# Kernel tuning notes

Hardware: AMD Instinct MI355X
Metric: run time of the kernel (lower is better)

The kernel has to match this reference:

```python
import jax, jax.numpy as jnp
import numpy as np

DIM, HEADS, HD = 256, 8, 32
WS, GT, SR = 8, 1, 2
B_, H0, W0 = 4, 128, 128
SCALE = HD ** -0.5


def _bilinear_up_align(x, s):
    # x: (B, C, h, w) -> (B, C, h*s, w*s), bilinear, align_corners=True (matches torch)
    B, C, h, w = x.shape
    oh, ow = h * s, w * s
    def coords(n, o):
        pos = jnp.arange(o, dtype=jnp.float32) * ((n - 1) / (o - 1))
        i0 = jnp.clip(jnp.floor(pos).astype(jnp.int32), 0, n - 2)
        t = pos - i0.astype(jnp.float32)
        return i0, t
    y0, ty = coords(h, oh)
    x0, tx = coords(w, ow)
    top = x[:, :, y0, :] * (1 - ty)[:, None] + x[:, :, y0 + 1, :] * ty[:, None]
    return top[:, :, :, x0] * (1 - tx) + top[:, :, :, x0 + 1] * tx


def _layernorm(x, w, b, eps=1e-5):
    mu = x.mean(-1, keepdims=True)
    var = x.var(-1, keepdims=True)
    return (x - mu) * jax.lax.rsqrt(var + eps) * w + b


def setup_inputs() -> dict:
    key = jax.random.key(0)
    ks = jax.random.split(key, 8)
    w = lambda k, shape: jax.random.normal(k, shape, jnp.float32) * 0.02
    return {
        "x": jax.random.normal(ks[0], (B_, H0 * W0, DIM), jnp.float32),
        "gt": jax.random.normal(ks[1], (B_, H0 // WS, W0 // WS, GT, DIM), jnp.float32),
        "q_w": w(ks[2], (DIM, DIM)), "q_b": jnp.zeros((DIM,), jnp.float32),
        "kv_w": w(ks[3], (2 * DIM, DIM)), "kv_b": jnp.zeros((2 * DIM,), jnp.float32),
        "sr_w": w(ks[4], (DIM, DIM, SR, SR)), "sr_b": jnp.zeros((DIM,), jnp.float32),
        "norm_w": jnp.ones((DIM,), jnp.float32), "norm_b": jnp.zeros((DIM,), jnp.float32),
        "proj_w": w(ks[5], (DIM, DIM)), "proj_b": jnp.zeros((DIM,), jnp.float32),
        "H": H0, "W": W0,
    }


def reference(x, gt, q_w, q_b, kv_w, kv_b, sr_w, sr_b, norm_w, norm_b, proj_w, proj_b, H, W):
    Bb, Np, C = x.shape
    nH, nW = H // WS, W // WS  # H, W multiples of WS -> no padding branch
    xm = x.reshape(Bb, H, W, C)
    # window partition -> (B, WS*WS, C), B = Bb*nH*nW
    xw = xm.reshape(Bb, nH, WS, nW, WS, C).transpose(0, 1, 3, 2, 4, 5).reshape(-1, WS * WS, C)
    g = gt.reshape(-1, GT, C)  # gt grid already matches (nH, nW)
    skip = g
    xc = jnp.concatenate([g, xw], axis=1)  # (B, N, C), N = GT + WS*WS
    B, N, _ = xc.shape
    q = (xc @ q_w.T + q_b).reshape(B, N, HEADS, HD).transpose(0, 2, 1, 3)  # (B,h,N,d)
    # spatial-reduction KV branch (sr_ratio > 1, gt_num != 0)
    x_ = xw.transpose(0, 2, 1).reshape(B, C, WS, WS)
    x_ = _bilinear_up_align(x_, SR)  # (B, C, WS*SR, WS*SR)
    x_ = jax.lax.conv_general_dilated(
        x_, sr_w, (SR, SR), "VALID",
        dimension_numbers=("NCHW", "OIHW", "NCHW")) + sr_b[None, :, None, None]  # (B,C,WS,WS)
    x_ = _layernorm(x_.reshape(B, C, -1).transpose(0, 2, 1), norm_w, norm_b)
    x_ = jnp.concatenate([g, x_], axis=1)  # (B, N, C)
    kv = (x_ @ kv_w.T + kv_b).reshape(B, -1, 2, HEADS, HD).transpose(2, 0, 3, 1, 4)
    k, v = kv[0], kv[1]  # (B,h,N,d)
    attn = jax.nn.softmax(jnp.einsum("bhnd,bhmd->bhnm", q, k) * SCALE, axis=-1)
    out = jnp.einsum("bhnm,bhmd->bhnd", attn, v).transpose(0, 2, 1, 3).reshape(B, N, C)
    out = out @ proj_w.T + proj_b
    gt_out = out[:, :GT, :]
    xo = out[:, GT:, :].reshape(Bb, nH, nW, WS, WS, C)
    xo = xo.transpose(0, 1, 3, 2, 4, 5).reshape(Bb, H, W, C)  # window reverse
    return xo.reshape(Bb, H * W, C), gt_out, skip
```

## Files before the change

kernel.cpp:

```cpp
#include <hip/hip_runtime.h>

typedef __attribute__((ext_vector_type(4))) float f32x4;
typedef __attribute__((ext_vector_type(8))) float f32x8;
typedef __attribute__((ext_vector_type(8))) short bf16x8;
typedef __attribute__((ext_vector_type(2))) uint u32x2;

#define SCALE_ 0.17677669529663687f

__device__ __forceinline__ float bf2f(ushort u){
  union { unsigned i; float f; } v; v.i = ((unsigned)u) << 16; return v.f;
}
__device__ __forceinline__ ushort f2bf(float f){
  union { float f; unsigned i; } v; v.f = f;
  unsigned r = v.i + 0x7fffu + ((v.i >> 16) & 1u);
  return (ushort)(r >> 16);
}
__device__ __forceinline__ void gl16(const void* g, const ushort* l) {
  __builtin_amdgcn_global_load_lds((const __attribute__((address_space(1))) uint*)g,
                                   (__attribute__((address_space(3))) uint*)l, 16, 0, 0);
}

__global__ __launch_bounds__(256) void k_prep(const float* __restrict__ x,
    const float* __restrict__ gt, const float* __restrict__ qw,
    const float* __restrict__ kvw, const float* __restrict__ pw,
    const float* __restrict__ srw, ushort* __restrict__ xc,
    ushort* __restrict__ xkv, float* __restrict__ out2,
    ushort* __restrict__ wq, ushort* __restrict__ wkv,
    ushort* __restrict__ wpr, ushort* __restrict__ wcv)
{
  int blk = blockIdx.x;
  int tid = threadIdx.x;
  if (blk >= 16640) {
    int i = (blk - 16640) * 256 + tid;
    if (i < 65536)            wq[i] = f2bf(qw[i]);
    else if (i < 196608)      wkv[i - 65536] = f2bf(kvw[i - 65536]);
    else if (i < 262144)      wpr[i - 196608] = f2bf(pw[i - 196608]);
    else {
      int j = i - 262144;
      int o = j >> 10, t = (j >> 8) & 3, cc = j & 255;
      wcv[j] = f2bf(srw[o * 1024 + cc * 4 + t]);
    }
    return;
  }
  int row = blk * 4 + (tid >> 6);
  int c4 = (tid & 63) * 4;
  int wi = row / 65, n = row - wi * 65;
  if (n == 0) {
    float4 g4 = *(const float4*)(gt + (size_t)wi * 256 + c4);
    uint lo = (uint)f2bf(g4.x) | ((uint)f2bf(g4.y) << 16);
    uint hi = (uint)f2bf(g4.z) | ((uint)f2bf(g4.w) << 16);
    u32x2 pk = {lo, hi};
    *(u32x2*)(xc  + (size_t)row * 256 + c4) = pk;
    *(u32x2*)(xkv + (size_t)row * 256 + c4) = pk;
    *(float4*)(out2 + (size_t)wi * 256 + c4) = g4;
  } else {
    int s = n - 1, r = s >> 3, cc = s & 7;
    int b = wi >> 8, wh = (wi >> 4) & 15, ww = wi & 15;
    int hw = (wh * 8 + r) * 128 + ww * 8 + cc;
    float4 v4 = *(const float4*)(x + ((size_t)b * 16384 + hw) * 256 + c4);
    uint lo = (uint)f2bf(v4.x) | ((uint)f2bf(v4.y) << 16);
    uint hi = (uint)f2bf(v4.z) | ((uint)f2bf(v4.w) << 16);
    u32x2 pk = {lo, hi};
    *(u32x2*)(xc + (size_t)row * 256 + c4) = pk;
  }
}

template<int N>
__global__ __launch_bounds__(256) void k_gemm2(const ushort* __restrict__ A,
    const ushort* __restrict__ W, const float* __restrict__ bias,
    ushort* __restrict__ C)
{
  constexpr int K = 256;
  __shared__ __align__(16) ushort As[2][128 * 64];
  __shared__ __align__(16) ushort Bs[2][128 * 64];
  int lin = blockIdx.y * gridDim.x + blockIdx.x;
  int qq = (gridDim.x * gridDim.y) >> 3;
  int sw2 = (lin & 7) * qq + (lin >> 3);
  int m0 = (sw2 / gridDim.x) * 128, n0 = (sw2 % gridDim.x) * 128;
  int tid = threadIdx.x, lane = tid & 63;
  int wave = tid >> 6;
  int lm = lane & 15, kg = lane >> 4;
  int wr = wave >> 1, wc = wave & 1;

  const char* Ab = (const char*)A + (size_t)m0 * (K * 2);
  const char* Bb = (const char*)W + (size_t)n0 * (K * 2);

  auto stage = [&](int buf, int kt) {
#pragma unroll
    for (int j = 0; j < 4; ++j) {
      int c = j * 256 + tid;
      int row = c >> 3, slot = c & 7;
      int srcoff = row * (K * 2) + kt * 128 + ((slot * 16) ^ ((row & 7) << 4));
      gl16(Ab + srcoff, (const ushort*)((const char*)As[buf] + c * 16));
      gl16(Bb + srcoff, (const ushort*)((const char*)Bs[buf] + c * 16));
    }
  };

  f32x4 acc[4][4];
  f32x4 zero = {0.f, 0.f, 0.f, 0.f};
#pragma unroll
  for (int a = 0; a < 4; ++a)
#pragma unroll
    for (int b = 0; b < 4; ++b) acc[a][b] = zero;

  stage(0, 0);
  __syncthreads();
#pragma unroll
  for (int t = 0; t < 4; ++t) {
    int cur = t & 1;
    if (t < 3) stage(cur ^ 1, t + 1);
#pragma unroll
    for (int s = 0; s < 2; ++s) {
      int sw = (lm & 7) << 4;
      bf16x8 af[4], bw[4];
#pragma unroll
      for (int mi = 0; mi < 4; ++mi) {
        int row = wr * 64 + mi * 16 + lm;
        af[mi] = *(const bf16x8*)((const char*)As[cur] + row * 128 + ((s * 64 + kg * 16) ^ sw));
      }
#pragma unroll
      for (int ni = 0; ni < 4; ++ni) {
        int row = wc * 64 + ni * 16 + lm;
        bw[ni] = *(const bf16x8*)((const char*)Bs[cur] + row * 128 + ((s * 64 + kg * 16) ^ sw));
      }
#pragma unroll
      for (int mi = 0; mi < 4; ++mi)
#pragma unroll
        for (int ni = 0; ni < 4; ++ni)
          acc[mi][ni] = __builtin_amdgcn_mfma_f32_16x16x32_bf16(af[mi], bw[ni], acc[mi][ni], 0, 0, 0);
    }
    __syncthreads();
  }

  int rbase = m0 + wr * 64 + kg * 4;
#pragma unroll
  for (int ni = 0; ni < 4; ++ni) {
    int col = n0 + wc * 64 + ni * 16 + lm;
    float bv = bias[col];
#pragma unroll
    for (int mi = 0; mi < 4; ++mi) {
#pragma unroll
      for (int r = 0; r < 4; ++r)
        C[(size_t)(rbase + mi * 16 + r) * N + col] = f2bf(acc[mi][ni][r] + bv);
    }
  }
}

__global__ __launch_bounds__(256) void k_gemm_out(const ushort* __restrict__ A,
    const ushort* __restrict__ W, const float* __restrict__ bias,
    float* __restrict__ out)
{
  constexpr int K = 256;
  __shared__ __align__(16) ushort As[2][128 * 64];
  __shared__ __align__(16) ushort Bs[2][128 * 64];
  int lin = blockIdx.y * gridDim.x + blockIdx.x;
  int qq = (gridDim.x * gridDim.y) >> 3;
  int sw2 = (lin & 7) * qq + (lin >> 3);
  int m0 = (sw2 / gridDim.x) * 128, n0 = (sw2 % gridDim.x) * 128;
  int tid = threadIdx.x, lane = tid & 63;
  int wave = tid >> 6;
  int lm = lane & 15, kg = lane >> 4;
  int wr = wave >> 1, wc = wave & 1;

  const char* Ab = (const char*)A + (size_t)m0 * (K * 2);
  const char* Bb = (const char*)W + (size_t)n0 * (K * 2);

  auto stage = [&](int buf, int kt) {
#pragma unroll
    for (int j = 0; j < 4; ++j) {
      int c = j * 256 + tid;
      int row = c >> 3, slot = c & 7;
      int srcoff = row * (K * 2) + kt * 128 + ((slot * 16) ^ ((row & 7) << 4));
      gl16(Ab + srcoff, (const ushort*)((const char*)As[buf] + c * 16));
      gl16(Bb + srcoff, (const ushort*)((const char*)Bs[buf] + c * 16));
    }
  };

  f32x4 acc[4][4];
  f32x4 zero = {0.f, 0.f, 0.f, 0.f};
#pragma unroll
  for (int a = 0; a < 4; ++a)
#pragma unroll
    for (int b = 0; b < 4; ++b) acc[a][b] = zero;

  stage(0, 0);
  __syncthreads();
#pragma unroll
  for (int t = 0; t < 4; ++t) {
    int cur = t & 1;
    if (t < 3) stage(cur ^ 1, t + 1);
#pragma unroll
    for (int s = 0; s < 2; ++s) {
      int sw = (lm & 7) << 4;
      bf16x8 af[4], bw[4];
#pragma unroll
      for (int mi = 0; mi < 4; ++mi) {
        int row = wr * 64 + mi * 16 + lm;
        af[mi] = *(const bf16x8*)((const char*)As[cur] + row * 128 + ((s * 64 + kg * 16) ^ sw));
      }
#pragma unroll
      for (int ni = 0; ni < 4; ++ni) {
        int row = wc * 64 + ni * 16 + lm;
        bw[ni] = *(const bf16x8*)((const char*)Bs[cur] + row * 128 + ((s * 64 + kg * 16) ^ sw));
      }
#pragma unroll
      for (int mi = 0; mi < 4; ++mi)
#pragma unroll
        for (int ni = 0; ni < 4; ++ni)
          acc[mi][ni] = __builtin_amdgcn_mfma_f32_16x16x32_bf16(af[mi], bw[ni], acc[mi][ni], 0, 0, 0);
    }
    __syncthreads();
  }

  int rbase = m0 + wr * 64 + kg * 4;
#pragma unroll
  for (int mi = 0; mi < 4; ++mi) {
#pragma unroll
    for (int r = 0; r < 4; ++r) {
      int g = rbase + mi * 16 + r;
      int wi2 = g / 65;
      int n = g - wi2 * 65;
      size_t dstrow;
      if (n == 0) {
        dstrow = (size_t)(16777216 >> 8) + wi2;
      } else {
        int s = n - 1;
        int b = wi2 >> 8, wh = (wi2 >> 4) & 15, ww = wi2 & 15;
        int r2 = s >> 3, cc = s & 7;
        dstrow = (size_t)(b << 14) + (wh * 8 + r2) * 128 + ww * 8 + cc;
      }
      float* dst = out + dstrow * 256;
#pragma unroll
      for (int ni = 0; ni < 4; ++ni) {
        int col = n0 + wc * 64 + ni * 16 + lm;
        dst[col] = acc[mi][ni][r] + bias[col];
      }
    }
  }
}

__global__ __launch_bounds__(512) void k_conv(const ushort* __restrict__ xc,
    const ushort* __restrict__ wconv, ushort* __restrict__ cconv)
{
  __shared__ ushort U[2][64 * 256];
  int wi = blockIdx.x;
  int tid = threadIdx.x, wave = tid >> 6, lane = tid & 63;
  int lm = lane & 15, kg = lane >> 4;
  const ushort* src = xc + (size_t)(wi * 65 + 1) * 256;
  f32x4 acc[4][2];
  f32x4 zero = {0.f, 0.f, 0.f, 0.f};
#pragma unroll
  for (int a = 0; a < 4; a++)
#pragma unroll
    for (int b = 0; b < 2; b++) acc[a][b] = zero;

  int cb = (tid & 31) * 8;
  int sg = tid >> 5;

  auto build = [&](int t, ushort* Ub) {
    int dy = t >> 1, dx = t & 1;
    for (int s = sg; s < 64; s += 16) {
      int i = s >> 3, j = s & 7;
      int yy = 2 * i + dy, xx = 2 * j + dx;
      float py = yy * (7.0f / 15.0f); int iy = (int)py; if (iy > 6) iy = 6; float ty = py - iy;
      float px = xx * (7.0f / 15.0f); int ix = (int)px; if (ix > 6) ix = 6; float tx = px - ix;
      float w00 = (1.f - ty) * (1.f - tx), w01 = (1.f - ty) * tx;
      float w10 = ty * (1.f - tx), w11 = ty * tx;
      const ushort* p = src + (size_t)(iy * 8 + ix) * 256 + cb;
      bf16x8 p00 = *(const bf16x8*)(p);
      bf16x8 p01 = *(const bf16x8*)(p + 256);
      bf16x8 p10 = *(const bf16x8*)(p + 2048);
      bf16x8 p11 = *(const bf16x8*)(p + 2304);
      bf16x8 o8;
#pragma unroll
      for (int jj = 0; jj < 8; jj++) {
        float v = w00 * bf2f((ushort)p00[jj]) + w01 * bf2f((ushort)p01[jj])
                + w10 * bf2f((ushort)p10[jj]) + w11 * bf2f((ushort)p11[jj]);
        o8[jj] = (short)f2bf(v);
      }
      int byteoff = s * 512 + ((2 * cb) ^ ((s & 7) << 4));
      *(bf16x8*)((char*)Ub + byteoff) = o8;
    }
  };

  build(0, U[0]);
  __syncthreads();
  for (int t = 0; t < 4; t++) {
    const ushort* Ub = U[t & 1];
    const ushort* wc = wconv + t * 256;
    for (int kk = 0; kk < 256; kk += 32) {
      int kb = kk + kg * 8;
      bf16x8 afr[4];
#pragma unroll
      for (int mi = 0; mi < 4; mi++) {
        int srow = mi * 16 + lm;
        int off = (srow * 512 + 2 * kb) ^ ((srow & 7) << 4);
        afr[mi] = *(const bf16x8*)((const char*)Ub + off);
      }
#pragma unroll
      for (int ni = 0; ni < 2; ni++) {
        bf16x8 b = *(const bf16x8*)(wc + (size_t)(wave * 32 + ni * 16 + lm) * 1024 + kb);
#pragma unroll
        for (int mi = 0; mi < 4; mi++)
          acc[mi][ni] = __builtin_amdgcn_mfma_f32_16x16x32_bf16(afr[mi], b, acc[mi][ni], 0, 0, 0);
      }
    }
    if (t < 3) build(t + 1, U[(t + 1) & 1]);
    __syncthreads();
  }

#pragma unroll
  for (int mi = 0; mi < 4; mi++) {
    int row = wi * 64 + mi * 16 + kg * 4;
#pragma unroll
    for (int ni = 0; ni < 2; ni++) {
      int col = wave * 32 + ni * 16 + lm;
#pragma unroll
      for (int r = 0; r < 4; r++)
        cconv[(size_t)(row + r) * 256 + col] = f2bf(acc[mi][ni][r]);
    }
  }
}

__global__ __launch_bounds__(256) void k_ln(const ushort* __restrict__ cconv,
    const float* __restrict__ srb, const float* __restrict__ nw,
    const float* __restrict__ nb, ushort* __restrict__ xkv)
{
  int row = blockIdx.x * 4 + (threadIdx.x >> 6);
  int lane = threadIdx.x & 63;
  int c0 = lane * 4;
  u32x2 pk = *(const u32x2*)(cconv + (size_t)row * 256 + c0);
  float4 sb4 = *(const float4*)(srb + c0);
  float v0 = bf2f((ushort)(pk.x & 0xffffu)) + sb4.x;
  float v1 = bf2f((ushort)(pk.x >> 16))     + sb4.y;
  float v2 = bf2f((ushort)(pk.y & 0xffffu)) + sb4.z;
  float v3 = bf2f((ushort)(pk.y >> 16))     + sb4.w;
  float sum = v0 + v1 + v2 + v3;
  float sq  = v0 * v0 + v1 * v1 + v2 * v2 + v3 * v3;
#pragma unroll
  for (int off = 1; off < 64; off <<= 1) {
    sum += __shfl_xor(sum, off, 64);
    sq  += __shfl_xor(sq,  off, 64);
  }
  float mean = sum * (1.f / 256.f);
  float var = sq * (1.f / 256.f) - mean * mean;
  float rs = rsqrtf(var + 1e-5f);
  float4 nw4 = *(const float4*)(nw + c0);
  float4 nb4 = *(const float4*)(nb + c0);
  int wi = row >> 6, s = row & 63;
  ushort* o = xkv + (size_t)(wi * 65 + 1 + s) * 256 + c0;
  uint lo = (uint)f2bf((v0 - mean) * rs * nw4.x + nb4.x)
          | ((uint)f2bf((v1 - mean) * rs * nw4.y + nb4.y) << 16);
  uint hi = (uint)f2bf((v2 - mean) * rs * nw4.z + nb4.z)
          | ((uint)f2bf((v3 - mean) * rs * nw4.w + nb4.w) << 16);
  u32x2 opk = {lo, hi};
  *(u32x2*)o = opk;
}

__global__ __launch_bounds__(256) void k_attn(const ushort* __restrict__ q,
    const ushort* __restrict__ kv, ushort* __restrict__ att)
{
  __shared__ ushort smem[4][8064];
  int wi = blockIdx.x >> 1;
  int tid = threadIdx.x, wave = tid >> 6, lane = tid & 63;
  int h = (blockIdx.x & 1) * 4 + wave;
  int lm = lane & 15, kg = lane >> 4;
  ushort* plds = smem[wave];
  ushort* vt   = smem[wave] + 5760;

  size_t qbase  = (size_t)wi * 65 * 256 + (size_t)h * 32;
  size_t kvbase = (size_t)wi * 65 * 512 + (size_t)h * 32;

  for (int e = lane; e < 2080; e += 64) {
    int m = e >> 5, d = e & 31;
    vt[d * 72 + m] = kv[kvbase + (size_t)m * 512 + 256 + d];
  }

  bf16x8 akf[5], bqf[5];
#pragma unroll
  for (int i = 0; i < 5; i++) {
    akf[i] = *(const bf16x8*)(kv + kvbase + (size_t)(16 * i + lm) * 512 + kg * 8);
    bqf[i] = *(const bf16x8*)(q  + qbase  + (size_t)(16 * i + lm) * 256 + kg * 8);
  }

  f32x4 sc[5][5];
  f32x4 zero = {0.f, 0.f, 0.f, 0.f};
#pragma unroll
  for (int mi = 0; mi < 5; mi++)
#pragma unroll
    for (int nj = 0; nj < 5; nj++) sc[mi][nj] = zero;
#pragma unroll
  for (int mi = 0; mi < 5; mi++)
#pragma unroll
    for (int nj = 0; nj < 5; nj++)
      sc[mi][nj] = __builtin_amdgcn_mfma_f32_16x16x32_bf16(akf[mi], bqf[nj], sc[mi][nj], 0, 0, 0);

  const float C = SCALE_ * 1.4426950408889634f;
  float inv[5], p64b[5];
#pragma unroll
  for (int nj = 0; nj < 5; nj++) {
    float s4 = sc[4][nj][0];
    float mx = (kg == 0) ? s4 : -1e30f;
#pragma unroll
    for (int mi = 0; mi < 4; mi++)
#pragma unroll
      for (int r = 0; r < 4; r++) mx = fmaxf(mx, sc[mi][nj][r]);
    mx = fmaxf(mx, __shfl_xor(mx, 16, 64));
    mx = fmaxf(mx, __shfl_xor(mx, 32, 64));
    float sum = 0.f;
#pragma unroll
    for (int mi = 0; mi < 4; mi++)
#pragma unroll
      for (int r = 0; r < 4; r++) {
        float e = exp2f((sc[mi][nj][r] - mx) * C);
        sc[mi][nj][r] = e; sum += e;
      }
    float e4 = exp2f((s4 - mx) * C);
    sum += (kg == 0) ? e4 : 0.f;
    sum += __shfl_xor(sum, 16, 64);
    sum += __shfl_xor(sum, 32, 64);
    inv[nj] = 1.0f / sum;
    p64b[nj] = __shfl(e4, lm, 64);
  }

#pragma unroll
  for (int nj = 0; nj < 5; nj++) {
    int n = 16 * nj + lm;
#pragma unroll
    for (int mi = 0; mi < 4; mi++) {
      uint lo = (uint)f2bf(sc[mi][nj][0]) | ((uint)f2bf(sc[mi][nj][1]) << 16);
      uint hi = (uint)f2bf(sc[mi][nj][2]) | ((uint)f2bf(sc[mi][nj][3]) << 16);
      u32x2 pk = {lo, hi};
      *(u32x2*)(plds + n * 72 + 16 * mi + 4 * kg) = pk;
    }
  }

  f32x4 od[2][5];
#pragma unroll
  for (int dt = 0; dt < 2; dt++)
#pragma unroll
    for (int nj = 0; nj < 5; nj++) od[dt][nj] = zero;
#pragma unroll
  for (int c = 0; c < 2; c++) {
    bf16x8 av[2], bp[5];
#pragma unroll
    for (int dt = 0; dt < 2; dt++)
      av[dt] = *(const bf16x8*)(vt + (16 * dt + lm) * 72 + c * 32 + kg * 8);
#pragma unroll
    for (int nj = 0; nj < 5; nj++)
      bp[nj] = *(const bf16x8*)(plds + (16 * nj + lm) * 72 + c * 32 + kg * 8);
#pragma unroll
    for (int dt = 0; dt < 2; dt++)
#pragma unroll
      for (int nj = 0; nj < 5; nj++)
        od[dt][nj] = __builtin_amdgcn_mfma_f32_16x16x32_bf16(av[dt], bp[nj], od[dt][nj], 0, 0, 0);
  }
  float v64[8];
#pragma unroll
  for (int dt = 0; dt < 2; dt++)
#pragma unroll
    for (int r = 0; r < 4; r++)
      v64[dt * 4 + r] = bf2f(vt[(16 * dt + 4 * kg + r) * 72 + 64]);
#pragma unroll
  for (int dt = 0; dt < 2; dt++)
#pragma unroll
    for (int nj = 0; nj < 5; nj++)
#pragma unroll
      for (int r = 0; r < 4; r++)
        od[dt][nj][r] += v64[dt * 4 + r] * p64b[nj];

#pragma unroll
  for (int nj = 0; nj < 5; nj++) {
    int n = 16 * nj + lm;
    float scl = inv[nj];
#pragma unroll
    for (int dt = 0; dt < 2; dt++) {
      uint lo = (uint)f2bf(od[dt][nj][0] * scl) | ((uint)f2bf(od[dt][nj][1] * scl) << 16);
      uint hi = (uint)f2bf(od[dt][nj][2] * scl) | ((uint)f2bf(od[dt][nj][3] * scl) << 16);
      u32x2 pk = {lo, hi};
      *(u32x2*)(plds + n * 40 + 16 * dt + 4 * kg) = pk;
    }
  }
  size_t abase = (size_t)wi * 65 * 256 + (size_t)h * 32;
  for (int e = lane; e < 1040; e += 64) {
    int n = e >> 4, d2 = e & 15;
    *(uint*)(att + abase + (size_t)n * 256 + 2 * d2) = *(const uint*)(plds + n * 40 + 2 * d2);
  }
}

extern "C" void kernel_launch(void* const* d_in, const int* in_sizes, int n_in,
                              void* d_out, int out_size, void* d_ws, size_t ws_size,
                              hipStream_t stream)
{
  const float* x    = (const float*)d_in[0];
  const float* gt   = (const float*)d_in[1];
  const float* q_w  = (const float*)d_in[2];
  const float* q_b  = (const float*)d_in[3];
  const float* kv_w = (const float*)d_in[4];
  const float* kv_b = (const float*)d_in[5];
  const float* sr_w = (const float*)d_in[6];
  const float* sr_b = (const float*)d_in[7];
  const float* nw   = (const float*)d_in[8];
  const float* nb   = (const float*)d_in[9];
  const float* p_w  = (const float*)d_in[10];
  const float* p_b  = (const float*)d_in[11];
  (void)in_sizes; (void)n_in; (void)out_size;

  if (ws_size < 204996608u) return;
  char* ws = (char*)d_ws;
  ushort* xc  = (ushort*)(ws);
  ushort* qb  = (ushort*)(ws + 34078720);
  ushort* xkv = (ushort*)(ws + 68157440);
  ushort* kv  = (ushort*)(ws + 102236160);
  ushort* ccv = (ushort*)(ws + 170393600);
  ushort* wq  = (ushort*)(ws + 203948032);
  ushort* wkv = (ushort*)(ws + 204079104);
  ushort* wpr = (ushort*)(ws + 204341248);
  ushort* wcv = (ushort*)(ws + 204472320);

  float* out = (float*)d_out;
  float* out2 = out + 16777216 + 262144;

  k_prep<<<18688, 256, 0, stream>>>(x, gt, q_w, kv_w, p_w, sr_w,
                                    xc, xkv, out2, wq, wkv, wpr, wcv);
  k_gemm2<256><<<dim3(2, 520), 256, 0, stream>>>(xc, wq, q_b, qb);
  k_conv<<<1024, 512, 0, stream>>>(xc, wcv, ccv);
  k_ln<<<16384, 256, 0, stream>>>(ccv, sr_b, nw, nb, xkv);
  k_gemm2<512><<<dim3(4, 520), 256, 0, stream>>>(xkv, wkv, kv_b, kv);
  k_attn<<<2048, 256, 0, stream>>>(qb, kv, xc);
  k_gemm_out<<<dim3(2, 520), 256, 0, stream>>>(xc, wpr, p_b, out);
}
```

Baseline: 240.1 us.

## Restructure conv kernel to 256 threads with half-K stages and smaller LDS

The spatial-reduction conv kernel now runs with 4 waves instead of 8, each wave covering 64 output columns. The K loop is split into 8 half-width stages of 128 channels, so the double-buffered LDS tile shrinks from 64 KB to 32 KB, which should allow more blocks resident per CU. The bilinear build gives each thread one fixed spatial position and 32 contiguous channels, hoisting the coordinate math out of the loop. In exchange there are more syncthreads, more accumulator registers per thread, and a changed LDS swizzle.

```diff
diff --git a/kernel.cpp b/kernel.cpp
--- a/kernel.cpp
+++ b/kernel.cpp
@@ -1,7 +1,6 @@
 #include <hip/hip_runtime.h>
 
 typedef __attribute__((ext_vector_type(4))) float f32x4;
-typedef __attribute__((ext_vector_type(8))) float f32x8;
 typedef __attribute__((ext_vector_type(8))) short bf16x8;
 typedef __attribute__((ext_vector_type(2))) uint u32x2;
 
@@ -239,73 +238,84 @@
   }
 }
 
-__global__ __launch_bounds__(512) void k_conv(const ushort* __restrict__ xc,
+__global__ __launch_bounds__(256) void k_conv(const ushort* __restrict__ xc,
     const ushort* __restrict__ wconv, ushort* __restrict__ cconv)
 {
-  __shared__ ushort U[2][64 * 256];
+  __shared__ __align__(16) ushort U2[2][64 * 128];
   int wi = blockIdx.x;
   int tid = threadIdx.x, wave = tid >> 6, lane = tid & 63;
   int lm = lane & 15, kg = lane >> 4;
   const ushort* src = xc + (size_t)(wi * 65 + 1) * 256;
-  f32x4 acc[4][2];
+
+  f32x4 acc[4][4];
   f32x4 zero = {0.f, 0.f, 0.f, 0.f};
 #pragma unroll
   for (int a = 0; a < 4; a++)
 #pragma unroll
-    for (int b = 0; b < 2; b++) acc[a][b] = zero;
-
-  int cb = (tid & 31) * 8;
-  int sg = tid >> 5;
-
-  auto build = [&](int t, ushort* Ub) {
+    for (int b = 0; b < 4; b++) acc[a][b] = zero;
+
+  int bs = tid >> 2, cq = tid & 3;
+  int bi = bs >> 3, bj = bs & 7;
+  float py = (2 * bi) * (7.0f / 15.0f);
+  float px = (2 * bj) * (7.0f / 15.0f);
+
+  auto build = [&](int st, ushort* Ub) {
+    int t = st >> 1, h = st & 1;
     int dy = t >> 1, dx = t & 1;
-    for (int s = sg; s < 64; s += 16) {
-      int i = s >> 3, j = s & 7;
-      int yy = 2 * i + dy, xx = 2 * j + dx;
-      float py = yy * (7.0f / 15.0f); int iy = (int)py; if (iy > 6) iy = 6; float ty = py - iy;
-      float px = xx * (7.0f / 15.0f); int ix = (int)px; if (ix > 6) ix = 6; float tx = px - ix;
-      float w00 = (1.f - ty) * (1.f - tx), w01 = (1.f - ty) * tx;
-      float w10 = ty * (1.f - tx), w11 = ty * tx;
-      const ushort* p = src + (size_t)(iy * 8 + ix) * 256 + cb;
-      bf16x8 p00 = *(const bf16x8*)(p);
-      bf16x8 p01 = *(const bf16x8*)(p + 256);
-      bf16x8 p10 = *(const bf16x8*)(p + 2048);
-      bf16x8 p11 = *(const bf16x8*)(p + 2304);
+    float pyt = py + dy * (7.0f / 15.0f);
+    float pxt = px + dx * (7.0f / 15.0f);
+    int iy = (int)pyt; if (iy > 6) iy = 6; float ty = pyt - iy;
+    int ix = (int)pxt; if (ix > 6) ix = 6; float tx = pxt - ix;
+    float w00 = (1.f - ty) * (1.f - tx), w01 = (1.f - ty) * tx;
+    float w10 = ty * (1.f - tx), w11 = ty * tx;
+    const ushort* p = src + (size_t)(iy * 8 + ix) * 256 + h * 128 + cq * 32;
+#pragma unroll
+    for (int j = 0; j < 4; ++j) {
+      bf16x8 p00 = *(const bf16x8*)(p + j * 8);
+      bf16x8 p01 = *(const bf16x8*)(p + j * 8 + 256);
+      bf16x8 p10 = *(const bf16x8*)(p + j * 8 + 2048);
+      bf16x8 p11 = *(const bf16x8*)(p + j * 8 + 2304);
       bf16x8 o8;
 #pragma unroll
-      for (int jj = 0; jj < 8; jj++) {
-        float v = w00 * bf2f((ushort)p00[jj]) + w01 * bf2f((ushort)p01[jj])
-                + w10 * bf2f((ushort)p10[jj]) + w11 * bf2f((ushort)p11[jj]);
-        o8[jj] = (short)f2bf(v);
-      }
-      int byteoff = s * 512 + ((2 * cb) ^ ((s & 7) << 4));
-      *(bf16x8*)((char*)Ub + byteoff) = o8;
+      for (int e = 0; e < 8; ++e) {
+        float v = w00 * bf2f((ushort)p00[e]) + w01 * bf2f((ushort)p01[e])
+                + w10 * bf2f((ushort)p10[e]) + w11 * bf2f((ushort)p11[e]);
+        o8[e] = (short)f2bf(v);
+      }
+      int colb = (cq * 32 + j * 8) * 2;
+      int addr = bs * 256 + (colb ^ ((bs & 15) << 4));
+      *(bf16x8*)((char*)Ub + addr) = o8;
     }
   };
 
-  build(0, U[0]);
-  __syncthreads();
-  for (int t = 0; t < 4; t++) {
-    const ushort* Ub = U[t & 1];
-    const ushort* wc = wconv + t * 256;
-    for (int kk = 0; kk < 256; kk += 32) {
-      int kb = kk + kg * 8;
+  auto mfma_st = [&](int st, const ushort* Ub) {
+    int t = st >> 1, h = st & 1;
+    const ushort* wc = wconv + t * 256 + h * 128;
+#pragma unroll
+    for (int kk = 0; kk < 128; kk += 32) {
+      int colb = 2 * (kk + kg * 8);
       bf16x8 afr[4];
 #pragma unroll
       for (int mi = 0; mi < 4; mi++) {
         int srow = mi * 16 + lm;
-        int off = (srow * 512 + 2 * kb) ^ ((srow & 7) << 4);
-        afr[mi] = *(const bf16x8*)((const char*)Ub + off);
-      }
-#pragma unroll
-      for (int ni = 0; ni < 2; ni++) {
-        bf16x8 b = *(const bf16x8*)(wc + (size_t)(wave * 32 + ni * 16 + lm) * 1024 + kb);
+        int addr = srow * 256 + (colb ^ ((srow & 15) << 4));
+        afr[mi] = *(const bf16x8*)((const char*)Ub + addr);
+      }
+#pragma unroll
+      for (int ni = 0; ni < 4; ni++) {
+        bf16x8 b = *(const bf16x8*)(wc + (size_t)(wave * 64 + ni * 16 + lm) * 1024 + kk + kg * 8);
 #pragma unroll
         for (int mi = 0; mi < 4; mi++)
           acc[mi][ni] = __builtin_amdgcn_mfma_f32_16x16x32_bf16(afr[mi], b, acc[mi][ni], 0, 0, 0);
       }
     }
-    if (t < 3) build(t + 1, U[(t + 1) & 1]);
+  };
+
+  build(0, U2[0]);
+  __syncthreads();
+  for (int st = 0; st < 8; ++st) {
+    mfma_st(st, U2[st & 1]);
+    if (st < 7) build(st + 1, U2[(st + 1) & 1]);
     __syncthreads();
   }
 
@@ -313,8 +323,8 @@
   for (int mi = 0; mi < 4; mi++) {
     int row = wi * 64 + mi * 16 + kg * 4;
 #pragma unroll
-    for (int ni = 0; ni < 2; ni++) {
-      int col = wave * 32 + ni * 16 + lm;
+    for (int ni = 0; ni < 4; ni++) {
+      int col = wave * 64 + ni * 16 + lm;
 #pragma unroll
       for (int r = 0; r < 4; r++)
         cconv[(size_t)(row + r) * 256 + col] = f2bf(acc[mi][ni][r]);
@@ -524,7 +534,7 @@
   k_prep<<<18688, 256, 0, stream>>>(x, gt, q_w, kv_w, p_w, sr_w,
                                     xc, xkv, out2, wq, wkv, wpr, wcv);
   k_gemm2<256><<<dim3(2, 520), 256, 0, stream>>>(xc, wq, q_b, qb);
-  k_conv<<<1024, 512, 0, stream>>>(xc, wcv, ccv);
+  k_conv<<<1024, 256, 0, stream>>>(xc, wcv, ccv);
   k_ln<<<16384, 256, 0, stream>>>(ccv, sr_b, nw, nb, xkv);
   k_gemm2<512><<<dim3(4, 520), 256, 0, stream>>>(xkv, wkv, kv_b, kv);
   k_attn<<<2048, 256, 0, stream>>>(qb, kv, xc);
```

After: 254.2 us. 5.9% more time.
